# Kernel tuning notes

Hardware: AMD Instinct MI355X
Metric: run time of the kernel (lower is better)

The kernel has to match this reference:

```python
import jax, jax.numpy as jnp
import numpy as np

SENTINEL = 24635
NUM_ENTITIES = 24636
EMB_DIM = 128


def setup_inputs() -> dict:
    key = jax.random.key(0)
    ks = jax.random.split(key, 6)
    B, L = 4096, 50
    return {
        "encoded_context_embs": jax.random.normal(ks[0], (B, 1024), jnp.float32),
        "ent_embs": jax.random.normal(ks[1], (NUM_ENTITIES, EMB_DIM), jnp.float32) * 0.02,
        "W1": jax.random.normal(ks[2], (768, 1024), jnp.float32) * 0.02,
        "W2": jax.random.normal(ks[3], (512, 768), jnp.float32) * 0.02,
        "W3": jax.random.normal(ks[4], (128, 512), jnp.float32) * 0.02,
        "ent_list": jax.random.randint(ks[5], (B, L), 0, NUM_ENTITIES, jnp.int64),
    }


def reference(encoded_context_embs, ent_embs, W1, W2, W3, ent_list):
    # --- ragged gather + masked mean with sentinel early-exit ---
    # valid[b, l] == 1 iff no sentinel appeared at positions <= l (prefix-AND)
    not_sent = (ent_list != SENTINEL).astype(ent_embs.dtype)   # [B, L]
    valid = jnp.cumprod(not_sent, axis=1)                      # [B, L]
    gathered = ent_embs[ent_list]                              # [B, L, D]
    cnt = valid.sum(axis=1)                                    # [B]
    summed = jnp.einsum("bl,bld->bd", valid, gathered)        # [B, D]
    mean = summed / jnp.maximum(cnt, 1.0)[:, None]
    # sentinel at position 0 -> fall back to the sentinel embedding
    user_embs = jnp.where((cnt == 0)[:, None], ent_embs[SENTINEL][None, :], mean)

    # --- MLP on pooled context: 1024 -> 768 -> 512 -> 128 ---
    x = jax.nn.relu(encoded_context_embs @ W1.T)
    x = jax.nn.relu(x @ W2.T)
    q = x @ W3.T                                               # [B, 128]

    # --- cross attention: query=q, key=value=user_embs ---
    scale = 1.0 / jnp.sqrt(jnp.asarray(q.shape[-1], q.dtype))
    scores = (q @ user_embs.T) * scale                         # [B, B]
    weights = jax.nn.softmax(scores, axis=-1)
    return weights @ user_embs                                 # [B, 128]
```

## Files before the change

kernel.cpp:

```cpp
#include <hip/hip_runtime.h>
#include <hip/hip_bf16.h>

#define SENTINEL 24635

using bf16x8  = __attribute__((ext_vector_type(8))) __bf16;
using bf16x2  = __attribute__((ext_vector_type(2))) __bf16;
using floatx4 = __attribute__((ext_vector_type(4))) float;

__device__ inline bf16x8 cvt8(float4 a, float4 b) {
  bf16x8 v;
  v[0] = (__bf16)a.x; v[1] = (__bf16)a.y; v[2] = (__bf16)a.z; v[3] = (__bf16)a.w;
  v[4] = (__bf16)b.x; v[5] = (__bf16)b.y; v[6] = (__bf16)b.z; v[7] = (__bf16)b.w;
  return v;
}

__device__ inline void gll16(const __bf16* g, __bf16* l) {
  __builtin_amdgcn_global_load_lds(
      (const __attribute__((address_space(1))) unsigned int*)g,
      (__attribute__((address_space(3))) unsigned int*)l, 16, 0, 0);
}

__global__ __launch_bounds__(256) void prep_kernel(
    const float* __restrict__ s0, __bf16* __restrict__ d0,
    const float* __restrict__ s1, __bf16* __restrict__ d1,
    const float* __restrict__ s2, __bf16* __restrict__ d2,
    const float* __restrict__ s3, __bf16* __restrict__ d3,
    const float* __restrict__ ent, const int* __restrict__ ent_list,
    __bf16* __restrict__ user_n) {
  if (blockIdx.x < 2656) {
    int g = blockIdx.x * 256 + threadIdx.x;
    const float* s; __bf16* d; int i;
    if (g < 524288)               { s = s0; d = d0; i = g; }
    else if (g < 622592)          { s = s1; d = d1; i = g - 524288; }
    else if (g < 671744)          { s = s2; d = d2; i = g - 622592; }
    else if (g < 679936)          { s = s3; d = d3; i = g - 671744; }
    else return;
    i *= 8;
    float4 a = *(const float4*)(s + i);
    float4 b = *(const float4*)(s + i + 4);
    *(bf16x8*)(d + i) = cvt8(a, b);
    return;
  }
  const int b = (blockIdx.x - 2656) * 4 + (threadIdx.x >> 6);
  const int lane = threadIdx.x & 63;
  int myidx = (lane < 50) ? ent_list[b * 50 + lane] : 0;
  unsigned long long m = __ballot(lane < 50 && myidx == SENTINEL);
  const int cnt = (m == 0) ? 50 : (int)__builtin_ctzll(m);

  float sx = 0.f, sy = 0.f;
  for (int l0 = 0; l0 < 50; l0 += 10) {
    if (l0 >= cnt) break;
    float2 e[10];
#pragma unroll
    for (int j = 0; j < 10; ++j) {
      int idx = __shfl(myidx, l0 + j);
      e[j] = *(const float2*)(ent + (size_t)idx * 128 + lane * 2);
    }
#pragma unroll
    for (int j = 0; j < 10; ++j) {
      if (l0 + j < cnt) { sx += e[j].x; sy += e[j].y; }
    }
  }
  float vx, vy;
  if (cnt == 0) {
    float2 e = *(const float2*)(ent + (size_t)SENTINEL * 128 + lane * 2);
    vx = e.x; vy = e.y;
  } else {
    float inv = 1.f / (float)cnt;
    vx = sx * inv; vy = sy * inv;
  }
  bf16x2 o; o[0] = (__bf16)vx; o[1] = (__bf16)vy;
  *(bf16x2*)(user_n + (size_t)b * 128 + lane * 2) = o;
}

template <int WR, int WC, int MT, int NT, int RELU>
__device__ inline void gemm_body(const __bf16* __restrict__ A,
                                 const __bf16* __restrict__ W,
                                 __bf16* __restrict__ C,
                                 int M, int N, int K, int bn0, int bm0,
                                 char* lds) {
  constexpr int BM = WR * MT * 16;
  constexpr int BN = WC * NT * 16;
  auto As = (__bf16 (*)[BM][32])lds;
  auto Bs = (__bf16 (*)[BN][32])(lds + (size_t)2 * BM * 32 * 2);
  const int tid  = threadIdx.x;
  const int w    = tid >> 6;
  const int lane = tid & 63;
  const int quad = lane >> 4;
  const int l16  = lane & 15;
  const int wr   = w / WC;
  const int wc   = w % WC;
  const int lrow = lane >> 2;
  const int lcol = (lane & 3) * 8;

  floatx4 acc[MT][NT];
#pragma unroll
  for (int mt = 0; mt < MT; ++mt)
#pragma unroll
    for (int nt = 0; nt < NT; ++nt) acc[mt][nt] = (floatx4){0.f, 0.f, 0.f, 0.f};

  constexpr int nAc = 2 * (BM / 16);
  constexpr int nBc = 2 * (BN / 16);
  for (int k0 = 0; k0 < K; k0 += 64) {
    __syncthreads();
#pragma unroll
    for (int c = w; c < nAc; c += 4) {
      int s = c / (BM / 16);
      int r = (c % (BM / 16)) * 16;
      gll16(A + (size_t)(bm0 + r + lrow) * K + k0 + s * 32 + lcol, &As[s][r][0]);
    }
#pragma unroll
    for (int c = w; c < nBc; c += 4) {
      int s = c / (BN / 16);
      int r = (c % (BN / 16)) * 16;
      gll16(W + (size_t)(bn0 + r + lrow) * K + k0 + s * 32 + lcol, &Bs[s][r][0]);
    }
    __syncthreads();
#pragma unroll
    for (int s = 0; s < 2; ++s) {
      bf16x8 af[MT], bfr[NT];
#pragma unroll
      for (int mt = 0; mt < MT; ++mt)
        af[mt] = *(const bf16x8*)&As[s][wr * (MT * 16) + mt * 16 + l16][quad * 8];
#pragma unroll
      for (int nt = 0; nt < NT; ++nt)
        bfr[nt] = *(const bf16x8*)&Bs[s][wc * (NT * 16) + nt * 16 + l16][quad * 8];
#pragma unroll
      for (int mt = 0; mt < MT; ++mt)
#pragma unroll
        for (int nt = 0; nt < NT; ++nt)
          acc[mt][nt] =
              __builtin_amdgcn_mfma_f32_16x16x32_bf16(af[mt], bfr[nt], acc[mt][nt], 0, 0, 0);
    }
  }

#pragma unroll
  for (int mt = 0; mt < MT; ++mt) {
    const int row0 = bm0 + wr * (MT * 16) + mt * 16 + quad * 4;
#pragma unroll
    for (int nt = 0; nt < NT; ++nt) {
      const int col = bn0 + wc * (NT * 16) + nt * 16 + l16;
#pragma unroll
      for (int r = 0; r < 4; ++r) {
        float v = acc[mt][nt][r];
        if (RELU) v = fmaxf(v, 0.f);
        C[(size_t)(row0 + r) * N + col] = (__bf16)v;
      }
    }
  }
}

template <int WR, int WC, int MT, int NT, int RELU>
__global__ __launch_bounds__(256) void gemm_bt(const __bf16* __restrict__ A,
                                               const __bf16* __restrict__ W,
                                               __bf16* __restrict__ C,
                                               int M, int N, int K) {
  __shared__ char lds[(size_t)2 * ((WR * MT * 16) + (WC * NT * 16)) * 32 * 2];
  gemm_body<WR, WC, MT, NT, RELU>(A, W, C, M, N, K,
                                  blockIdx.x * (WC * NT * 16),
                                  blockIdx.y * (WR * MT * 16), lds);
}

__global__ __launch_bounds__(256) void gemm1_tr(const __bf16* __restrict__ A,
                                                const __bf16* __restrict__ W,
                                                __bf16* __restrict__ C,
                                                const __bf16* __restrict__ un,
                                                __bf16* __restrict__ ut) {
  __shared__ char lds[16384];
  const int bx = blockIdx.x;
  if (bx < 768) {
    gemm_body<2, 2, 2, 2, 1>(A, W, C, 4096, 768, 1024,
                             (bx % 12) * 64, (bx / 12) * 64, lds);
    return;
  }
  const int idx = bx - 768;
  const int r0 = (idx & 63) * 64;
  const int c0 = (idx >> 6) * 64;
  auto T = (__bf16 (*)[72])lds;
  const int tid = threadIdx.x;
#pragma unroll
  for (int p = 0; p < 2; ++p) {
    int r = (tid >> 3) + p * 32;
    int c = (tid & 7) * 8;
    *(bf16x8*)&T[r][c] = *(const bf16x8*)(un + (size_t)(r0 + r) * 128 + c0 + c);
  }
  __syncthreads();
#pragma unroll
  for (int p = 0; p < 2; ++p) {
    int c = (tid >> 3) + p * 32;
    int r = (tid & 7) * 8;
    bf16x8 v;
#pragma unroll
    for (int j = 0; j < 8; ++j) v[j] = T[r + j][c];
    *(bf16x8*)(ut + (size_t)(c0 + c) * 4096 + r0 + r) = v;
  }
}

__global__ __launch_bounds__(256) void flash_attn(const __bf16* __restrict__ Q,
                                                  const __bf16* __restrict__ Un_g,
                                                  const __bf16* __restrict__ Ut_g,
                                                  __bf16* __restrict__ O_part,
                                                  float* __restrict__ lp) {
  __shared__ __bf16 Un[64][136];
  __shared__ __bf16 Ut[128][72];
  __shared__ __bf16 Ps[4][16][72];
  const int tid  = threadIdx.x;
  const int w    = tid >> 6;
  const int lane = tid & 63;
  const int quad = lane >> 4;
  const int l16  = lane & 15;
  const int qrow0 = blockIdx.x * 64;
  const int split = blockIdx.y;
  const float scale = 0.08838834764831845f;

  bf16x8 aq[4];
#pragma unroll
  for (int c = 0; c < 4; ++c)
    aq[c] = *(const bf16x8*)(Q + (size_t)(qrow0 + w * 16 + l16) * 128 + c * 32 + quad * 8);

  floatx4 o[8];
#pragma unroll
  for (int t = 0; t < 8; ++t) o[t] = (floatx4){0.f, 0.f, 0.f, 0.f};
  float lsum[4] = {0.f, 0.f, 0.f, 0.f};

  for (int chunk = 0; chunk < 4; ++chunk) {
    const int key0 = split * 256 + chunk * 64;
    __syncthreads();
#pragma unroll
    for (int p = 0; p < 4; ++p) {
      int r = (tid >> 4) + p * 16;
      int c = (tid & 15) * 8;
      *(bf16x8*)&Un[r][c] = *(const bf16x8*)(Un_g + (size_t)(key0 + r) * 128 + c);
    }
#pragma unroll
    for (int p = 0; p < 4; ++p) {
      int d = (tid >> 3) + p * 32;
      int kk = (tid & 7) * 8;
      *(bf16x8*)&Ut[d][kk] = *(const bf16x8*)(Ut_g + (size_t)d * 4096 + key0 + kk);
    }
    __syncthreads();

#pragma unroll
    for (int t = 0; t < 4; ++t) {
      floatx4 s = (floatx4){0.f, 0.f, 0.f, 0.f};
#pragma unroll
      for (int c = 0; c < 4; ++c) {
        bf16x8 bk = *(const bf16x8*)&Un[t * 16 + l16][c * 32 + quad * 8];
        s = __builtin_amdgcn_mfma_f32_16x16x32_bf16(aq[c], bk, s, 0, 0, 0);
      }
#pragma unroll
      for (int r = 0; r < 4; ++r) {
        float pv = __expf(s[r] * scale);
        lsum[r] += pv;
        Ps[w][quad * 4 + r][t * 16 + l16] = (__bf16)pv;
      }
    }

#pragma unroll
    for (int c2 = 0; c2 < 2; ++c2) {
      bf16x8 ap = *(const bf16x8*)&Ps[w][l16][c2 * 32 + quad * 8];
#pragma unroll
      for (int dt = 0; dt < 8; ++dt) {
        bf16x8 bv = *(const bf16x8*)&Ut[dt * 16 + l16][c2 * 32 + quad * 8];
        o[dt] = __builtin_amdgcn_mfma_f32_16x16x32_bf16(ap, bv, o[dt], 0, 0, 0);
      }
    }
  }

#pragma unroll
  for (int r = 0; r < 4; ++r) {
    float v = lsum[r];
    v += __shfl_xor(v, 1);
    v += __shfl_xor(v, 2);
    v += __shfl_xor(v, 4);
    v += __shfl_xor(v, 8);
    lsum[r] = v;
  }

  __bf16* Ob = O_part + (size_t)split * 4096 * 128;
  const int row0 = qrow0 + w * 16 + quad * 4;
#pragma unroll
  for (int dt = 0; dt < 8; ++dt) {
#pragma unroll
    for (int r = 0; r < 4; ++r) {
      Ob[(size_t)(row0 + r) * 128 + dt * 16 + l16] = (__bf16)o[dt][r];
    }
  }
  if (l16 == 0) {
#pragma unroll
    for (int r = 0; r < 4; ++r) lp[(size_t)(row0 + r) * 16 + split] = lsum[r];
  }
}

__global__ __launch_bounds__(256) void combine_kernel(const __bf16* __restrict__ Op,
                                                      const float* __restrict__ lp,
                                                      float* __restrict__ out) {
  const int i = (blockIdx.x * 256 + threadIdx.x) * 8;
  const int row = i >> 7;
  float num[8] = {0.f, 0.f, 0.f, 0.f, 0.f, 0.f, 0.f, 0.f};
#pragma unroll
  for (int s = 0; s < 16; ++s) {
    bf16x8 v = *(const bf16x8*)(Op + (size_t)s * 524288 + i);
#pragma unroll
    for (int j = 0; j < 8; ++j) num[j] += (float)v[j];
  }
  float den = 0.f;
#pragma unroll
  for (int j = 0; j < 4; ++j) {
    float4 d4 = *(const float4*)(lp + (size_t)row * 16 + j * 4);
    den += d4.x + d4.y + d4.z + d4.w;
  }
  float inv = 1.f / den;
  float4 r0 = {num[0] * inv, num[1] * inv, num[2] * inv, num[3] * inv};
  float4 r1 = {num[4] * inv, num[5] * inv, num[6] * inv, num[7] * inv};
  *(float4*)(out + i) = r0;
  *(float4*)(out + i + 4) = r1;
}

extern "C" void kernel_launch(void* const* d_in, const int* in_sizes, int n_in,
                              void* d_out, int out_size, void* d_ws, size_t ws_size,
                              hipStream_t stream) {
  (void)in_sizes; (void)n_in; (void)out_size; (void)ws_size;
  const float* ctx      = (const float*)d_in[0];
  const float* ent_embs = (const float*)d_in[1];
  const float* W1       = (const float*)d_in[2];
  const float* W2       = (const float*)d_in[3];
  const float* W3       = (const float*)d_in[4];
  const int*   ent_list = (const int*)d_in[5];
  float* out = (float*)d_out;

  char* base = (char*)d_ws;
  __bf16* user_n = (__bf16*)(base);
  __bf16* user_t = (__bf16*)(base + (1ull << 20));
  __bf16* qb     = (__bf16*)(base + (2ull << 20));
  float*  lp     = (float*)(base + (3ull << 20));
  __bf16* ctxb   = (__bf16*)(base + (4ull << 20));
  __bf16* W1b    = (__bf16*)(base + (12ull << 20));
  __bf16* W2b    = (__bf16*)(base + 14155776ull);
  __bf16* W3b    = (__bf16*)(base + 14942208ull);
  __bf16* x1b    = (__bf16*)(base + (15ull << 20));
  __bf16* x2b    = (__bf16*)(base + (21ull << 20));
  __bf16* O_part = (__bf16*)(base + (25ull << 20));

  prep_kernel<<<3680, 256, 0, stream>>>(ctx, ctxb, W1, W1b, W2, W2b, W3, W3b,
                                        ent_embs, ent_list, user_n);
  gemm1_tr<<<896, 256, 0, stream>>>(ctxb, W1b, x1b, user_n, user_t);
  gemm_bt<2, 2, 2, 2, 1><<<dim3(8, 64), 256, 0, stream>>>(x1b, W2b, x2b, 4096, 512, 768);
  gemm_bt<2, 2, 1, 1, 0><<<dim3(4, 128), 256, 0, stream>>>(x2b, W3b, qb, 4096, 128, 512);
  flash_attn<<<dim3(64, 16), 256, 0, stream>>>(qb, user_n, user_t, O_part, lp);
  combine_kernel<<<256, 256, 0, stream>>>(O_part, lp, out);
}
```

Before: 169.6 us.

## Fuse all stages into one persistent kernel with software grid barriers

Replaces six separate kernel launches with a single persistent 512-block kernel. The stages (conversion and pooling, three GEMMs with the transpose, flash attention, combine) are separated by atomic-counter grid barriers. Tile shapes and split counts are also re-chosen to fit the fixed grid: 8 attention splits instead of 16, and a wider GEMM1 tile. The intent is to remove launch gaps and inter-kernel idle time. The cost is that it relies on all 512 blocks being co-resident (2 per CU), adds barrier spin overhead, and gives fewer blocks per stage, which can reduce parallelism in the GEMM and attention phases.

```diff
diff --git a/kernel.cpp b/kernel.cpp
--- a/kernel.cpp
+++ b/kernel.cpp
@@ -4,6 +4,7 @@
 #define SENTINEL 24635
 
 using bf16x8  = __attribute__((ext_vector_type(8))) __bf16;
+using bf16x4  = __attribute__((ext_vector_type(4))) __bf16;
 using bf16x2  = __attribute__((ext_vector_type(2))) __bf16;
 using floatx4 = __attribute__((ext_vector_type(4))) float;
 
@@ -20,57 +21,16 @@
       (__attribute__((address_space(3))) unsigned int*)l, 16, 0, 0);
 }
 
-__global__ __launch_bounds__(256) void prep_kernel(
-    const float* __restrict__ s0, __bf16* __restrict__ d0,
-    const float* __restrict__ s1, __bf16* __restrict__ d1,
-    const float* __restrict__ s2, __bf16* __restrict__ d2,
-    const float* __restrict__ s3, __bf16* __restrict__ d3,
-    const float* __restrict__ ent, const int* __restrict__ ent_list,
-    __bf16* __restrict__ user_n) {
-  if (blockIdx.x < 2656) {
-    int g = blockIdx.x * 256 + threadIdx.x;
-    const float* s; __bf16* d; int i;
-    if (g < 524288)               { s = s0; d = d0; i = g; }
-    else if (g < 622592)          { s = s1; d = d1; i = g - 524288; }
-    else if (g < 671744)          { s = s2; d = d2; i = g - 622592; }
-    else if (g < 679936)          { s = s3; d = d3; i = g - 671744; }
-    else return;
-    i *= 8;
-    float4 a = *(const float4*)(s + i);
-    float4 b = *(const float4*)(s + i + 4);
-    *(bf16x8*)(d + i) = cvt8(a, b);
-    return;
-  }
-  const int b = (blockIdx.x - 2656) * 4 + (threadIdx.x >> 6);
-  const int lane = threadIdx.x & 63;
-  int myidx = (lane < 50) ? ent_list[b * 50 + lane] : 0;
-  unsigned long long m = __ballot(lane < 50 && myidx == SENTINEL);
-  const int cnt = (m == 0) ? 50 : (int)__builtin_ctzll(m);
-
-  float sx = 0.f, sy = 0.f;
-  for (int l0 = 0; l0 < 50; l0 += 10) {
-    if (l0 >= cnt) break;
-    float2 e[10];
-#pragma unroll
-    for (int j = 0; j < 10; ++j) {
-      int idx = __shfl(myidx, l0 + j);
-      e[j] = *(const float2*)(ent + (size_t)idx * 128 + lane * 2);
-    }
-#pragma unroll
-    for (int j = 0; j < 10; ++j) {
-      if (l0 + j < cnt) { sx += e[j].x; sy += e[j].y; }
-    }
-  }
-  float vx, vy;
-  if (cnt == 0) {
-    float2 e = *(const float2*)(ent + (size_t)SENTINEL * 128 + lane * 2);
-    vx = e.x; vy = e.y;
-  } else {
-    float inv = 1.f / (float)cnt;
-    vx = sx * inv; vy = sy * inv;
-  }
-  bf16x2 o; o[0] = (__bf16)vx; o[1] = (__bf16)vy;
-  *(bf16x2*)(user_n + (size_t)b * 128 + lane * 2) = o;
+__device__ inline void grid_barrier(unsigned* c, unsigned target) {
+  __syncthreads();
+  if (threadIdx.x == 0) {
+    __threadfence();
+    __hip_atomic_fetch_add(c, 1u, __ATOMIC_RELEASE, __HIP_MEMORY_SCOPE_AGENT);
+    while (__hip_atomic_load(c, __ATOMIC_RELAXED, __HIP_MEMORY_SCOPE_AGENT) < target)
+      __builtin_amdgcn_s_sleep(4);
+    (void)__hip_atomic_load(c, __ATOMIC_ACQUIRE, __HIP_MEMORY_SCOPE_AGENT);
+  }
+  __syncthreads();
 }
 
 template <int WR, int WC, int MT, int NT, int RELU>
@@ -150,171 +110,215 @@
   }
 }
 
-template <int WR, int WC, int MT, int NT, int RELU>
-__global__ __launch_bounds__(256) void gemm_bt(const __bf16* __restrict__ A,
-                                               const __bf16* __restrict__ W,
-                                               __bf16* __restrict__ C,
-                                               int M, int N, int K) {
-  __shared__ char lds[(size_t)2 * ((WR * MT * 16) + (WC * NT * 16)) * 32 * 2];
-  gemm_body<WR, WC, MT, NT, RELU>(A, W, C, M, N, K,
-                                  blockIdx.x * (WC * NT * 16),
-                                  blockIdx.y * (WR * MT * 16), lds);
-}
-
-__global__ __launch_bounds__(256) void gemm1_tr(const __bf16* __restrict__ A,
-                                                const __bf16* __restrict__ W,
-                                                __bf16* __restrict__ C,
-                                                const __bf16* __restrict__ un,
-                                                __bf16* __restrict__ ut) {
-  __shared__ char lds[16384];
-  const int bx = blockIdx.x;
-  if (bx < 768) {
-    gemm_body<2, 2, 2, 2, 1>(A, W, C, 4096, 768, 1024,
-                             (bx % 12) * 64, (bx / 12) * 64, lds);
-    return;
-  }
-  const int idx = bx - 768;
-  const int r0 = (idx & 63) * 64;
-  const int c0 = (idx >> 6) * 64;
-  auto T = (__bf16 (*)[72])lds;
-  const int tid = threadIdx.x;
-#pragma unroll
-  for (int p = 0; p < 2; ++p) {
-    int r = (tid >> 3) + p * 32;
-    int c = (tid & 7) * 8;
-    *(bf16x8*)&T[r][c] = *(const bf16x8*)(un + (size_t)(r0 + r) * 128 + c0 + c);
-  }
-  __syncthreads();
-#pragma unroll
-  for (int p = 0; p < 2; ++p) {
-    int c = (tid >> 3) + p * 32;
-    int r = (tid & 7) * 8;
-    bf16x8 v;
-#pragma unroll
-    for (int j = 0; j < 8; ++j) v[j] = T[r + j][c];
-    *(bf16x8*)(ut + (size_t)(c0 + c) * 4096 + r0 + r) = v;
-  }
-}
-
-__global__ __launch_bounds__(256) void flash_attn(const __bf16* __restrict__ Q,
-                                                  const __bf16* __restrict__ Un_g,
-                                                  const __bf16* __restrict__ Ut_g,
-                                                  __bf16* __restrict__ O_part,
-                                                  float* __restrict__ lp) {
-  __shared__ __bf16 Un[64][136];
-  __shared__ __bf16 Ut[128][72];
-  __shared__ __bf16 Ps[4][16][72];
+__global__ __launch_bounds__(256, 2) void mega_kernel(
+    const float* __restrict__ ctx, const float* __restrict__ ent,
+    const int* __restrict__ ent_list,
+    const float* __restrict__ W1, const float* __restrict__ W2,
+    const float* __restrict__ W3,
+    __bf16* __restrict__ ctxb, __bf16* __restrict__ W1b,
+    __bf16* __restrict__ W2b, __bf16* __restrict__ W3b,
+    __bf16* __restrict__ user_n, __bf16* __restrict__ user_t,
+    __bf16* __restrict__ x1b, __bf16* __restrict__ x2b,
+    __bf16* __restrict__ qb, __bf16* __restrict__ O_part,
+    float* __restrict__ lp, float* __restrict__ out,
+    unsigned* ctr) {
+  __shared__ char lds[46080];
   const int tid  = threadIdx.x;
+  const int bid  = blockIdx.x;
   const int w    = tid >> 6;
   const int lane = tid & 63;
   const int quad = lane >> 4;
   const int l16  = lane & 15;
-  const int qrow0 = blockIdx.x * 64;
-  const int split = blockIdx.y;
-  const float scale = 0.08838834764831845f;
-
-  bf16x8 aq[4];
-#pragma unroll
-  for (int c = 0; c < 4; ++c)
-    aq[c] = *(const bf16x8*)(Q + (size_t)(qrow0 + w * 16 + l16) * 128 + c * 32 + quad * 8);
-
-  floatx4 o[8];
-#pragma unroll
-  for (int t = 0; t < 8; ++t) o[t] = (floatx4){0.f, 0.f, 0.f, 0.f};
-  float lsum[4] = {0.f, 0.f, 0.f, 0.f};
-
-  for (int chunk = 0; chunk < 4; ++chunk) {
-    const int key0 = split * 256 + chunk * 64;
+
+  {
+    const int gid = bid * 256 + tid;
+    for (int u = gid; u < 679936; u += 131072) {
+      const float* s; __bf16* d; int i;
+      if (u < 524288)      { s = ctx; d = ctxb; i = u; }
+      else if (u < 622592) { s = W1;  d = W1b;  i = u - 524288; }
+      else if (u < 671744) { s = W2;  d = W2b;  i = u - 622592; }
+      else                 { s = W3;  d = W3b;  i = u - 671744; }
+      i *= 8;
+      float4 a = *(const float4*)(s + i);
+      float4 b = *(const float4*)(s + i + 4);
+      *(bf16x8*)(d + i) = cvt8(a, b);
+    }
+    for (int rr = 0; rr < 2; ++rr) {
+      const int b = bid * 8 + w * 2 + rr;
+      int myidx = (lane < 50) ? ent_list[b * 50 + lane] : 0;
+      unsigned long long m = __ballot(lane < 50 && myidx == SENTINEL);
+      const int cnt = (m == 0) ? 50 : (int)__builtin_ctzll(m);
+      float sx = 0.f, sy = 0.f;
+      for (int l0 = 0; l0 < 50; l0 += 10) {
+        if (l0 >= cnt) break;
+        float2 e[10];
+#pragma unroll
+        for (int j = 0; j < 10; ++j) {
+          int idx = __shfl(myidx, l0 + j);
+          e[j] = *(const float2*)(ent + (size_t)idx * 128 + lane * 2);
+        }
+#pragma unroll
+        for (int j = 0; j < 10; ++j) {
+          if (l0 + j < cnt) { sx += e[j].x; sy += e[j].y; }
+        }
+      }
+      float vx, vy;
+      if (cnt == 0) {
+        float2 e = *(const float2*)(ent + (size_t)SENTINEL * 128 + lane * 2);
+        vx = e.x; vy = e.y;
+      } else {
+        float inv = 1.f / (float)cnt;
+        vx = sx * inv; vy = sy * inv;
+      }
+      bf16x2 o; o[0] = (__bf16)vx; o[1] = (__bf16)vy;
+      *(bf16x2*)(user_n + (size_t)b * 128 + lane * 2) = o;
+    }
+  }
+  grid_barrier(ctr + 0, 512);
+
+  gemm_body<2, 2, 2, 3, 1>(ctxb, W1b, x1b, 4096, 768, 1024,
+                           (bid % 8) * 96, (bid / 8) * 64, lds);
+  grid_barrier(ctr + 1, 512);
+
+  gemm_body<2, 2, 2, 2, 1>(x1b, W2b, x2b, 4096, 512, 768,
+                           (bid % 8) * 64, (bid / 8) * 64, lds);
+  grid_barrier(ctr + 2, 512);
+
+  if (bid < 256) {
+    gemm_body<2, 2, 1, 2, 0>(x2b, W3b, qb, 4096, 128, 512,
+                             (bid % 2) * 64, (bid / 2) * 32, lds);
+  } else if (bid < 384) {
+    const int idx = bid - 256;
+    const int r0 = (idx & 63) * 64;
+    const int c0 = (idx >> 6) * 64;
+    auto T = (__bf16 (*)[72])lds;
     __syncthreads();
 #pragma unroll
-    for (int p = 0; p < 4; ++p) {
-      int r = (tid >> 4) + p * 16;
-      int c = (tid & 15) * 8;
-      *(bf16x8*)&Un[r][c] = *(const bf16x8*)(Un_g + (size_t)(key0 + r) * 128 + c);
-    }
-#pragma unroll
-    for (int p = 0; p < 4; ++p) {
-      int d = (tid >> 3) + p * 32;
-      int kk = (tid & 7) * 8;
-      *(bf16x8*)&Ut[d][kk] = *(const bf16x8*)(Ut_g + (size_t)d * 4096 + key0 + kk);
+    for (int p = 0; p < 2; ++p) {
+      int r = (tid >> 3) + p * 32;
+      int c = (tid & 7) * 8;
+      *(bf16x8*)&T[r][c] = *(const bf16x8*)(user_n + (size_t)(r0 + r) * 128 + c0 + c);
     }
     __syncthreads();
-
-#pragma unroll
-    for (int t = 0; t < 4; ++t) {
-      floatx4 s = (floatx4){0.f, 0.f, 0.f, 0.f};
-#pragma unroll
-      for (int c = 0; c < 4; ++c) {
-        bf16x8 bk = *(const bf16x8*)&Un[t * 16 + l16][c * 32 + quad * 8];
-        s = __builtin_amdgcn_mfma_f32_16x16x32_bf16(aq[c], bk, s, 0, 0, 0);
-      }
+#pragma unroll
+    for (int p = 0; p < 2; ++p) {
+      int c = (tid >> 3) + p * 32;
+      int r = (tid & 7) * 8;
+      bf16x8 v;
+#pragma unroll
+      for (int j = 0; j < 8; ++j) v[j] = T[r + j][c];
+      *(bf16x8*)(user_t + (size_t)(c0 + c) * 4096 + r0 + r) = v;
+    }
+  }
+  grid_barrier(ctr + 3, 512);
+
+  {
+    auto Un = (__bf16 (*)[136])lds;
+    auto Ut = (__bf16 (*)[72])(lds + 17408);
+    auto Ps = (__bf16 (*)[16][72])(lds + 35840);
+    const int qrow0 = (bid >> 3) * 64;
+    const int split = bid & 7;
+    const float scale = 0.08838834764831845f;
+
+    bf16x8 aq[4];
+#pragma unroll
+    for (int c = 0; c < 4; ++c)
+      aq[c] = *(const bf16x8*)(qb + (size_t)(qrow0 + w * 16 + l16) * 128 + c * 32 + quad * 8);
+
+    floatx4 o[8];
+#pragma unroll
+    for (int t = 0; t < 8; ++t) o[t] = (floatx4){0.f, 0.f, 0.f, 0.f};
+    float lsum[4] = {0.f, 0.f, 0.f, 0.f};
+
+    for (int chunk = 0; chunk < 8; ++chunk) {
+      const int key0 = split * 512 + chunk * 64;
+      __syncthreads();
+#pragma unroll
+      for (int p = 0; p < 4; ++p) {
+        int r = (tid >> 4) + p * 16;
+        int c = (tid & 15) * 8;
+        *(bf16x8*)&Un[r][c] = *(const bf16x8*)(user_n + (size_t)(key0 + r) * 128 + c);
+      }
+#pragma unroll
+      for (int p = 0; p < 4; ++p) {
+        int d = (tid >> 3) + p * 32;
+        int kk = (tid & 7) * 8;
+        *(bf16x8*)&Ut[d][kk] = *(const bf16x8*)(user_t + (size_t)d * 4096 + key0 + kk);
+      }
+      __syncthreads();
+
+#pragma unroll
+      for (int t = 0; t < 4; ++t) {
+        floatx4 s = (floatx4){0.f, 0.f, 0.f, 0.f};
+#pragma unroll
+        for (int c = 0; c < 4; ++c) {
+          bf16x8 bk = *(const bf16x8*)&Un[t * 16 + l16][c * 32 + quad * 8];
+          s = __builtin_amdgcn_mfma_f32_16x16x32_bf16(aq[c], bk, s, 0, 0, 0);
+        }
+#pragma unroll
+        for (int r = 0; r < 4; ++r) {
+          float pv = __expf(s[r] * scale);
+          lsum[r] += pv;
+          Ps[w][quad * 4 + r][t * 16 + l16] = (__bf16)pv;
+        }
+      }
+
+#pragma unroll
+      for (int c2 = 0; c2 < 2; ++c2) {
+        bf16x8 ap = *(const bf16x8*)&Ps[w][l16][c2 * 32 + quad * 8];
+#pragma unroll
+        for (int dt = 0; dt < 8; ++dt) {
+          bf16x8 bv = *(const bf16x8*)&Ut[dt * 16 + l16][c2 * 32 + quad * 8];
+          o[dt] = __builtin_amdgcn_mfma_f32_16x16x32_bf16(ap, bv, o[dt], 0, 0, 0);
+        }
+      }
+    }
+
+#pragma unroll
+    for (int r = 0; r < 4; ++r) {
+      float v = lsum[r];
+      v += __shfl_xor(v, 1);
+      v += __shfl_xor(v, 2);
+      v += __shfl_xor(v, 4);
+      v += __shfl_xor(v, 8);
+      lsum[r] = v;
+    }
+
+    __bf16* Ob = O_part + (size_t)split * 524288;
+    const int row0 = qrow0 + w * 16 + quad * 4;
+#pragma unroll
+    for (int dt = 0; dt < 8; ++dt) {
 #pragma unroll
       for (int r = 0; r < 4; ++r) {
-        float pv = __expf(s[r] * scale);
-        lsum[r] += pv;
-        Ps[w][quad * 4 + r][t * 16 + l16] = (__bf16)pv;
-      }
-    }
-
-#pragma unroll
-    for (int c2 = 0; c2 < 2; ++c2) {
-      bf16x8 ap = *(const bf16x8*)&Ps[w][l16][c2 * 32 + quad * 8];
-#pragma unroll
-      for (int dt = 0; dt < 8; ++dt) {
-        bf16x8 bv = *(const bf16x8*)&Ut[dt * 16 + l16][c2 * 32 + quad * 8];
-        o[dt] = __builtin_amdgcn_mfma_f32_16x16x32_bf16(ap, bv, o[dt], 0, 0, 0);
-      }
-    }
-  }
-
-#pragma unroll
-  for (int r = 0; r < 4; ++r) {
-    float v = lsum[r];
-    v += __shfl_xor(v, 1);
-    v += __shfl_xor(v, 2);
-    v += __shfl_xor(v, 4);
-    v += __shfl_xor(v, 8);
-    lsum[r] = v;
-  }
-
-  __bf16* Ob = O_part + (size_t)split * 4096 * 128;
-  const int row0 = qrow0 + w * 16 + quad * 4;
-#pragma unroll
-  for (int dt = 0; dt < 8; ++dt) {
-#pragma unroll
-    for (int r = 0; r < 4; ++r) {
-      Ob[(size_t)(row0 + r) * 128 + dt * 16 + l16] = (__bf16)o[dt][r];
-    }
-  }
-  if (l16 == 0) {
-#pragma unroll
-    for (int r = 0; r < 4; ++r) lp[(size_t)(row0 + r) * 16 + split] = lsum[r];
-  }
-}
-
-__global__ __launch_bounds__(256) void combine_kernel(const __bf16* __restrict__ Op,
-                                                      const float* __restrict__ lp,
-                                                      float* __restrict__ out) {
-  const int i = (blockIdx.x * 256 + threadIdx.x) * 8;
-  const int row = i >> 7;
-  float num[8] = {0.f, 0.f, 0.f, 0.f, 0.f, 0.f, 0.f, 0.f};
-#pragma unroll
-  for (int s = 0; s < 16; ++s) {
-    bf16x8 v = *(const bf16x8*)(Op + (size_t)s * 524288 + i);
-#pragma unroll
-    for (int j = 0; j < 8; ++j) num[j] += (float)v[j];
-  }
-  float den = 0.f;
-#pragma unroll
-  for (int j = 0; j < 4; ++j) {
-    float4 d4 = *(const float4*)(lp + (size_t)row * 16 + j * 4);
-    den += d4.x + d4.y + d4.z + d4.w;
-  }
-  float inv = 1.f / den;
-  float4 r0 = {num[0] * inv, num[1] * inv, num[2] * inv, num[3] * inv};
-  float4 r1 = {num[4] * inv, num[5] * inv, num[6] * inv, num[7] * inv};
-  *(float4*)(out + i) = r0;
-  *(float4*)(out + i + 4) = r1;
+        Ob[(size_t)(row0 + r) * 128 + dt * 16 + l16] = (__bf16)o[dt][r];
+      }
+    }
+    if (l16 == 0) {
+#pragma unroll
+      for (int r = 0; r < 4; ++r) lp[(size_t)(row0 + r) * 8 + split] = lsum[r];
+    }
+  }
+  grid_barrier(ctr + 4, 512);
+
+  {
+    const int gid = bid * 256 + tid;
+    const int i = gid * 4;
+    const int row = i >> 7;
+    float num[4] = {0.f, 0.f, 0.f, 0.f};
+#pragma unroll
+    for (int s = 0; s < 8; ++s) {
+      bf16x4 v = *(const bf16x4*)(O_part + (size_t)s * 524288 + i);
+#pragma unroll
+      for (int j = 0; j < 4; ++j) num[j] += (float)v[j];
+    }
+    float den = 0.f;
+    float4 d0 = *(const float4*)(lp + (size_t)row * 8);
+    float4 d1 = *(const float4*)(lp + (size_t)row * 8 + 4);
+    den = d0.x + d0.y + d0.z + d0.w + d1.x + d1.y + d1.z + d1.w;
+    float inv = 1.f / den;
+    float4 r0 = {num[0] * inv, num[1] * inv, num[2] * inv, num[3] * inv};
+    *(float4*)(out + i) = r0;
+  }
 }
 
 extern "C" void kernel_launch(void* const* d_in, const int* in_sizes, int n_in,
@@ -341,12 +345,10 @@
   __bf16* x1b    = (__bf16*)(base + (15ull << 20));
   __bf16* x2b    = (__bf16*)(base + (21ull << 20));
   __bf16* O_part = (__bf16*)(base + (25ull << 20));
-
-  prep_kernel<<<3680, 256, 0, stream>>>(ctx, ctxb, W1, W1b, W2, W2b, W3, W3b,
-                                        ent_embs, ent_list, user_n);
-  gemm1_tr<<<896, 256, 0, stream>>>(ctxb, W1b, x1b, user_n, user_t);
-  gemm_bt<2, 2, 2, 2, 1><<<dim3(8, 64), 256, 0, stream>>>(x1b, W2b, x2b, 4096, 512, 768);
-  gemm_bt<2, 2, 1, 1, 0><<<dim3(4, 128), 256, 0, stream>>>(x2b, W3b, qb, 4096, 128, 512);
-  flash_attn<<<dim3(64, 16), 256, 0, stream>>>(qb, user_n, user_t, O_part, lp);
-  combine_kernel<<<256, 256, 0, stream>>>(O_part, lp, out);
-}
+  unsigned* ctr  = (unsigned*)(base + (250ull << 20));
+
+  hipMemsetAsync(ctr, 0, 32, stream);
+  mega_kernel<<<512, 256, 0, stream>>>(ctx, ent_embs, ent_list, W1, W2, W3,
+                                       ctxb, W1b, W2b, W3b, user_n, user_t,
+                                       x1b, x2b, qb, O_part, lp, out, ctr);
+}
```

Measured after the change: 434.7 us. 156% more time.
